# Kernel tuning notes

Hardware: AMD Instinct MI355X
Metric: run time of the kernel (lower is better)

## Reference

```python
import jax, jax.numpy as jnp
import numpy as np

# JetBlock dims
B, T, HID = 2, 2048, 2048
H, DK, DV = 16, 128, 128
W = 4                      # dynamic short-conv kernel size
GEN_IN = 2 * H * DK        # kernel generator conditioned on concat(q, k)
GEN_HID = H * DV
EPS_NORM = 1e-6
EPS_L2 = 1e-12


def _silu(x):
    return x * jax.nn.sigmoid(x)


def setup_inputs() -> dict:
    key = jax.random.key(0)
    ks = jax.random.split(key, 12)
    s = 0.02
    return {
        "x": jax.random.normal(ks[0], (B, T, HID), jnp.float32),
        "Wq": jax.random.normal(ks[1], (HID, H * DK), jnp.float32) * s,
        "Wk": jax.random.normal(ks[2], (HID, H * DK), jnp.float32) * s,
        "Wv": jax.random.normal(ks[3], (HID, H * DV), jnp.float32) * s,
        "Wb": jax.random.normal(ks[4], (HID, H), jnp.float32) * s,
        "Wa": jax.random.normal(ks[5], (HID, H), jnp.float32) * s,
        "dt_bias": jax.random.normal(ks[6], (H,), jnp.float32) * s,
        "A_log": jax.random.normal(ks[7], (H,), jnp.float32) * 0.5,
        "gen_w1": jax.random.normal(ks[8], (GEN_IN, GEN_HID), jnp.float32) * s,
        "gen_w2": jax.random.normal(ks[9], (GEN_HID, H * DV * W), jnp.float32) * s,
        "gen_b2": jnp.zeros((H * DV * W,), jnp.float32),
        "norm_weight": jnp.ones((DV,), jnp.float32),
        "Wg": jax.random.normal(ks[10], (HID, H * DV), jnp.float32) * s,
        "Wo": jax.random.normal(ks[11], (H * DV, HID), jnp.float32) * s,
    }


def reference(x, Wq, Wk, Wv, Wb, Wa, dt_bias, A_log, gen_w1, gen_w2, gen_b2,
              norm_weight, Wg, Wo):
    # projections
    q = (x @ Wq).reshape(B, T, H, DK)
    k = (x @ Wk).reshape(B, T, H, DK)
    v = x @ Wv  # [B, T, H*DV]

    # dynamic short convolution on v, kernels generated from concat(q, k)
    gi = jnp.concatenate([q.reshape(B, T, -1), k.reshape(B, T, -1)], axis=-1)
    kern = (_silu(gi @ gen_w1) @ gen_w2 + gen_b2).reshape(B, T, H * DV, W)
    vp = jnp.pad(v, ((0, 0), (W - 1, 0), (0, 0)))  # causal left pad
    # out[t, d] = sum_w kern[t, d, w] * v[t - (W-1) + w, d]
    vconv = kern[..., 0] * vp[:, 0:T, :]
    for w in range(1, W):
        vconv = vconv + kern[..., w] * vp[:, w:w + T, :]
    v = _silu(vconv).reshape(B, T, H, DV)

    # gating params (gated-deltanet parameterization)
    beta = jax.nn.sigmoid(x @ Wb)                              # [B, T, H]
    g = -jnp.exp(A_log) * jax.nn.softplus(x @ Wa + dt_bias)    # log-space decay <= 0
    decay = jnp.exp(g)

    # qk l2 norm (F.normalize semantics)
    qn = q / jnp.maximum(jnp.linalg.norm(q, axis=-1, keepdims=True), EPS_L2)
    kn = k / jnp.maximum(jnp.linalg.norm(k, axis=-1, keepdims=True), EPS_L2)

    # gated delta rule recurrence (o_t reads state BEFORE the update, per source)
    def step(S, inps):
        q_t, k_t, v_t, g_t, b_t = inps
        o_t = jnp.einsum('bnkv,bnk->bnv', S, q_t)
        Sk = jnp.einsum('bnkv,bnk->bnv', S, k_t)
        delta = v_t - Sk
        S = g_t[..., None, None] * S + b_t[..., None, None] * (
            k_t[..., :, None] * delta[..., None, :])
        return S, o_t

    S0 = jnp.zeros((B, H, DK, DV), x.dtype)
    xs = (jnp.moveaxis(qn, 1, 0), jnp.moveaxis(kn, 1, 0), jnp.moveaxis(v, 1, 0),
          jnp.moveaxis(decay, 1, 0), jnp.moveaxis(beta, 1, 0))
    _, o = jax.lax.scan(step, S0, xs)           # o: [T, B, H, DV]
    o = jnp.moveaxis(o, 0, 1)                   # [B, T, H, DV]

    # gated RMSNorm per head, then output projection
    gate = (x @ Wg).reshape(B, T, H, DV)
    rms = o * jax.lax.rsqrt(jnp.mean(o * o, axis=-1, keepdims=True) + EPS_NORM)
    o = rms * norm_weight * _silu(gate)
    return o.reshape(B, T, H * DV) @ Wo
```

## Files before the change

### kernel.cpp

```cpp
#include <hip/hip_runtime.h>
#include <hip/hip_bf16.h>


typedef _Float16 v8h __attribute__((ext_vector_type(8)));
typedef _Float16 v4h __attribute__((ext_vector_type(4)));
typedef _Float16 v2h __attribute__((ext_vector_type(2)));
typedef float    v4f __attribute__((ext_vector_type(4)));

__device__ __forceinline__ void gload16(const void* g, void* l) {
  __builtin_amdgcn_global_load_lds(
      (const __attribute__((address_space(1))) unsigned int*)g,
      (__attribute__((address_space(3))) unsigned int*)l, 16, 0, 0);
}

__global__ __launch_bounds__(256)
void transpose_cast(const float* __restrict__ src, _Float16* __restrict__ dst,
                    int R, int C)
{
  __shared__ float tile[32][33];
  int c0 = blockIdx.x * 32, r0 = blockIdx.y * 32;
  int tx = threadIdx.x & 31, ty = threadIdx.x >> 5;
  #pragma unroll
  for (int i = 0; i < 32; i += 8)
    tile[ty + i][tx] = src[(size_t)(r0 + ty + i) * C + c0 + tx];
  __syncthreads();
  #pragma unroll
  for (int i = 0; i < 32; i += 8)
    dst[(size_t)(c0 + ty + i) * R + r0 + tx] = (_Float16)tile[tx][ty + i];
}

__global__ __launch_bounds__(256)
void cast_f32_f16(const float* __restrict__ src, _Float16* __restrict__ dst, int n4)
{
  int i = blockIdx.x * 256 + threadIdx.x;
  if (i >= n4) return;
  float4 v = ((const float4*)src)[i];
  v4h h = {(_Float16)v.x, (_Float16)v.y, (_Float16)v.z, (_Float16)v.w};
  *(v4h*)&dst[4 * (size_t)i] = h;
}

template<int MODE>
__global__ __launch_bounds__(512, 2)
void gemm256(const _Float16* __restrict__ A, const _Float16* __restrict__ Bt,
             void* __restrict__ Cout, const float* __restrict__ bias,
             int M, int N, int K)
{
  __shared__ _Float16 lds[65536];
  const int tid  = threadIdx.x;
  const int lane = tid & 63;
  const int wid  = tid >> 6;
  const int wm   = wid >> 2;
  const int wn   = wid & 3;
  const int l16  = lane & 15;
  const int q8   = (lane >> 4) * 8;
  const int swzx = (l16 & 7) << 3;

  const int nbx = N >> 8;
  const int cpx = gridDim.x >> 3;
  const int swz = (blockIdx.x & 7) * cpx + (blockIdx.x >> 3);
  const int bm0 = (swz / nbx) << 8;
  const int bn0 = (swz % nbx) << 8;

  const _Float16* Abase = A  + (size_t)bm0 * K;
  const _Float16* Bbase = Bt + (size_t)bn0 * K;

  const int r0 = tid >> 3;
  const int cs = ((tid & 7) * 8) ^ ((r0 & 7) << 3);

#define SLOTA(par, half) (lds + ((par) * 2 + (half)) * 8192)
#define SLOTB(par, half) (lds + 32768 + ((par) * 2 + (half)) * 8192)
#define STAGE(basep, kt, slot) do {                                        \
    _Float16* sst_ = (slot);                                               \
    gload16((basep) + (size_t)r0 * K + (kt) + cs, sst_ + tid * 8);         \
    gload16((basep) + (size_t)(r0 + 64) * K + (kt) + cs,                   \
            sst_ + 4096 + tid * 8);                                        \
  } while (0)
#define LOADA(par, mh) do {                                                \
    const _Float16* sld_ = SLOTA(par, mh);                                 \
    _Pragma("unroll")                                                      \
    for (int ks = 0; ks < 2; ks++)                                         \
      _Pragma("unroll")                                                    \
      for (int mi = 0; mi < 4; mi++)                                       \
        af[ks][mi] = *(const v8h*)&sld_[(wm * 64 + mi * 16 + l16) * 64 +   \
                                        ((ks * 32 + q8) ^ swzx)];          \
  } while (0)
#define LOADB(par, nh) do {                                                \
    const _Float16* sld_ = SLOTB(par, nh);                                 \
    _Pragma("unroll")                                                      \
    for (int ks = 0; ks < 2; ks++)                                         \
      _Pragma("unroll")                                                    \
      for (int ni = 0; ni < 2; ni++)                                       \
        bf[ks][ni] = *(const v8h*)&sld_[(wn * 32 + ni * 16 + l16) * 64 +   \
                                        ((ks * 32 + q8) ^ swzx)];          \
  } while (0)
#define MMAC(mh, nh) do {                                                  \
    __builtin_amdgcn_s_setprio(1);                                         \
    _Pragma("unroll")                                                      \
    for (int ks = 0; ks < 2; ks++)                                         \
      _Pragma("unroll")                                                    \
      for (int mi = 0; mi < 4; mi++)                                       \
        _Pragma("unroll")                                                  \
        for (int ni = 0; ni < 2; ni++)                                     \
          acc[mh][mi][nh][ni] = __builtin_amdgcn_mfma_f32_16x16x32_f16(    \
              af[ks][mi], bf[ks][ni], acc[mh][mi][nh][ni], 0, 0, 0);       \
    __builtin_amdgcn_s_setprio(0);                                         \
  } while (0)

  v4f acc[2][4][2][2];
  #pragma unroll
  for (int mh = 0; mh < 2; mh++)
    #pragma unroll
    for (int mi = 0; mi < 4; mi++)
      #pragma unroll
      for (int nh = 0; nh < 2; nh++)
        #pragma unroll
        for (int ni = 0; ni < 2; ni++)
          acc[mh][mi][nh][ni] = v4f{0.f, 0.f, 0.f, 0.f};
  v8h af[2][4], bf[2][2];

  const int nt = K >> 6;

  STAGE(Abase,                   0,  SLOTA(0, 0));
  STAGE(Bbase,                   0,  SLOTB(0, 0));
  STAGE(Abase + (size_t)128 * K, 0,  SLOTA(0, 1));
  STAGE(Bbase + (size_t)128 * K, 0,  SLOTB(0, 1));
  STAGE(Abase,                   64, SLOTA(1, 0));
  STAGE(Bbase + (size_t)128 * K, 64, SLOTB(1, 1));
  asm volatile("s_waitcnt vmcnt(4)" ::: "memory");
  __builtin_amdgcn_s_barrier();

  for (int T = 0; T < nt; T++) {
    const int par = T & 1;
    const int kt1 = (T + 1) << 6;
    const int kt2 = (T + 2) << 6;
    LOADA(par, 0);
    LOADB(par, 0);
    if (T + 1 < nt) STAGE(Abase + (size_t)128 * K, kt1, SLOTA(par ^ 1, 1));
    __builtin_amdgcn_s_barrier();
    MMAC(0, 0);
    __builtin_amdgcn_s_barrier();
    LOADB(par, 1);
    if (T + 1 < nt) STAGE(Bbase, kt1, SLOTB(par ^ 1, 0));
    __builtin_amdgcn_s_barrier();
    MMAC(0, 1);
    __builtin_amdgcn_s_barrier();
    LOADA(par, 1);
    if (T + 2 < nt) STAGE(Abase, kt2, SLOTA(par, 0));
    __builtin_amdgcn_s_barrier();
    MMAC(1, 1);
    __builtin_amdgcn_s_barrier();
    LOADB(par, 0);
    if (T + 2 < nt) STAGE(Bbase + (size_t)128 * K, kt2, SLOTB(par, 1));
    __builtin_amdgcn_s_barrier();
    MMAC(1, 0);
    if (T + 2 < nt) { asm volatile("s_waitcnt vmcnt(4)" ::: "memory"); }
    else            { asm volatile("s_waitcnt vmcnt(0)" ::: "memory"); }
    __builtin_amdgcn_s_barrier();
  }

  const int q4 = (lane >> 4) * 4;
  #pragma unroll
  for (int mh = 0; mh < 2; mh++) {
    #pragma unroll
    for (int mi = 0; mi < 4; mi++) {
      #pragma unroll
      for (int nh = 0; nh < 2; nh++) {
        #pragma unroll
        for (int ni = 0; ni < 2; ni++) {
          const int gn = bn0 + nh * 128 + wn * 32 + ni * 16 + l16;
          #pragma unroll
          for (int r = 0; r < 4; r++) {
            const int gm = bm0 + mh * 128 + wm * 64 + mi * 16 + q4 + r;
            float val = acc[mh][mi][nh][ni][r];
            size_t offc = (size_t)gm * N + gn;
            if (MODE == 0) {
              ((float*)Cout)[offc] = val;
            } else if (MODE == 1) {
              float s = val / (1.0f + expf(-val));
              ((_Float16*)Cout)[offc] = (_Float16)s;
            } else if (MODE == 2) {
              float s = val + bias[gn];
              ((_Float16*)Cout)[offc] = (_Float16)s;
            } else {
              ((_Float16*)Cout)[offc] = (_Float16)val;
            }
          }
        }
      }
    }
  }
#undef SLOTA
#undef SLOTB
#undef STAGE
#undef LOADA
#undef LOADB
#undef MMAC
}

__global__ __launch_bounds__(256)
void conv_silu(const _Float16* __restrict__ vg, const _Float16* __restrict__ kernc,
               float* __restrict__ vprime, int chunk)
{
  int idx = blockIdx.x * 256 + threadIdx.x;
  int btl = idx >> 11;
  int d   = idx & 2047;
  int btg = chunk * 2048 + btl;
  v4h kv = *(const v4h*)&kernc[(size_t)btl * 8192 + d * 4];
  float kw0 = (float)kv[0], kw1 = (float)kv[1], kw2 = (float)kv[2], kw3 = (float)kv[3];
  const _Float16* vcol = vg + d;
  float acc = kw3 * (float)vcol[(size_t)btg * 4096];
  if (btl >= 1) acc += kw2 * (float)vcol[(size_t)(btg - 1) * 4096];
  if (btl >= 2) acc += kw1 * (float)vcol[(size_t)(btg - 2) * 4096];
  if (btl >= 3) acc += kw0 * (float)vcol[(size_t)(btg - 3) * 4096];
  vprime[(size_t)btg * 2048 + d] = acc / (1.0f + expf(-acc));
}

__global__ __launch_bounds__(256)
void beta_decay(const float* __restrict__ x, const float* __restrict__ Wb,
                const float* __restrict__ Wa, const float* __restrict__ dt_bias,
                const float* __restrict__ A_log,
                float* __restrict__ beta, float* __restrict__ glog)
{
  __shared__ float xs[2048];
  __shared__ float red[8][32];
  int row = blockIdx.x;
  int tid = threadIdx.x;
  for (int i = tid; i < 2048; i += 256) xs[i] = x[(size_t)row * 2048 + i];
  __syncthreads();
  int j = tid & 31, kg = tid >> 5;
  const float* W = (j < 16) ? Wb : Wa;
  int jj = j & 15;
  float acc = 0.f;
  int k0 = kg * 256;
  for (int k = k0; k < k0 + 256; k++) acc += xs[k] * W[(size_t)k * 16 + jj];
  red[kg][j] = acc;
  __syncthreads();
  if (tid < 32) {
    float s = 0.f;
    #pragma unroll
    for (int g2 = 0; g2 < 8; g2++) s += red[g2][tid];
    int hh = tid & 15;
    if (tid < 16) {
      beta[(size_t)row * 16 + hh] = 1.0f / (1.0f + expf(-s));
    } else {
      float tt = s + dt_bias[hh];
      float sp = (tt > 20.f) ? tt : log1pf(expf(tt));
      glog[(size_t)row * 16 + hh] = -expf(A_log[hh]) * sp;
    }
  }
}

__global__ __launch_bounds__(256)
void recurrence_seg(const _Float16* __restrict__ gi,
                    const float* __restrict__ vprime,
                    const float* __restrict__ betab,
                    const float* __restrict__ glogb,
                    float* __restrict__ o,
                    float* __restrict__ Send,
                    _Float16* __restrict__ obasis)
{
  __shared__ _Float16 Q16[32][136];
  __shared__ _Float16 K16[32][136];
  __shared__ _Float16 KT16[2][128][40];
  __shared__ _Float16 St16[64][136];
  __shared__ float V32[32][68];
  __shared__ float W0L[32][65];
  __shared__ float O0L[32][65];
  __shared__ float At32[32][32];
  __shared__ _Float16 B16[32][40];
  __shared__ _Float16 Ut16[64][40];
  __shared__ _Float16 Utp16[64][40];
  __shared__ float lgA[2][32], lgm1A[2][32], gm1E[2][32], bGA[2][32],
                   psA[2][32], betA[2][32], p31A[2];

  const int tid  = threadIdx.x;
  const int wid  = tid >> 6;
  const int lane = tid & 63;
  const int l16  = lane & 15;
  const int q8   = (lane >> 4) * 8;
  const int q4   = (lane >> 4) * 4;
  const int rg   = lane >> 4;
  const int wc   = wid * 16 + l16;

  const int role = blockIdx.x >> 6;
  const int blk  = blockIdx.x & 63;
  const int dvh  = blk & 1;
  const int h    = (blk >> 1) & 15;
  const int b    = blk >> 5;
  const int tbase = (role == 0) ? 0 : 1024;
  const bool basis = (role == 2);

  const _Float16* gq = gi + (size_t)b * 2048 * 4096 + h * 128;
  const _Float16* gk = gq + 2048;
  const float* vsrc = vprime + (size_t)b * 2048 * 2048 + h * 128 + dvh * 64;
  float* ob = o + ((size_t)(b * 2048 + tbase) * 16 + h) * 128 + dvh * 64;
  _Float16* obb = obasis + ((size_t)b * 1024 * 16 + h) * 128 + dvh * 64;

  const int sr  = tid >> 3;
  const int sc8 = tid & 7;
  const int c0  = sc8 * 16;
  const int ktsw = (tid & 3) << 3;

  v4f sfr[8];
  #pragma unroll
  for (int tn = 0; tn < 8; tn++) {
    #pragma unroll
    for (int fr = 0; fr < 4; fr++)
      sfr[tn][fr] = (basis && (tn * 16 + l16) == (dvh * 64 + wid * 16 + q4 + fr))
                        ? 1.f : 0.f;
  }

  v8h pq0, pq1, pk0, pk1;
  float4 pv0 = {0.f, 0.f, 0.f, 0.f}, pv1 = {0.f, 0.f, 0.f, 0.f};
  float pg = 0.f, pb = 0.f;

  auto stage_regs = [&](int t0) {
    pq0 = *(const v8h*)(gq + (size_t)(t0 + sr) * 4096 + c0);
    pq1 = *(const v8h*)(gq + (size_t)(t0 + sr) * 4096 + c0 + 8);
    pk0 = *(const v8h*)(gk + (size_t)(t0 + sr) * 4096 + c0);
    pk1 = *(const v8h*)(gk + (size_t)(t0 + sr) * 4096 + c0 + 8);
    if (!basis) {
      pv0 = *(const float4*)(vsrc + (size_t)(t0 + sr) * 2048 + sc8 * 8);
      pv1 = *(const float4*)(vsrc + (size_t)(t0 + sr) * 2048 + sc8 * 8 + 4);
    }
    if (tid < 32) {
      size_t bt_ = (size_t)(b * 2048 + t0 + tid) * 16 + h;
      pg = glogb[bt_];
      pb = betab[bt_];
    }
  };

  auto write_stage = [&](int pn) {
    float qf[16], kf[16];
    #pragma unroll
    for (int m = 0; m < 8; m++) {
      qf[m] = (float)pq0[m]; qf[m + 8] = (float)pq1[m];
      kf[m] = (float)pk0[m]; kf[m + 8] = (float)pk1[m];
    }
    float ssq = 0.f, ssk = 0.f;
    #pragma unroll
    for (int m = 0; m < 16; m++) { ssq += qf[m] * qf[m]; ssk += kf[m] * kf[m]; }
    ssq += __shfl_xor(ssq, 1); ssq += __shfl_xor(ssq, 2); ssq += __shfl_xor(ssq, 4);
    ssk += __shfl_xor(ssk, 1); ssk += __shfl_xor(ssk, 2); ssk += __shfl_xor(ssk, 4);
    float iq = 1.0f / fmaxf(sqrtf(ssq), 1e-12f);
    float ik = 1.0f / fmaxf(sqrtf(ssk), 1e-12f);
    v8h qo0, qo1, ko0, ko1;
    #pragma unroll
    for (int m = 0; m < 8; m++) {
      qo0[m] = (_Float16)(qf[m] * iq); qo1[m] = (_Float16)(qf[m + 8] * iq);
      ko0[m] = (_Float16)(kf[m] * ik); ko1[m] = (_Float16)(kf[m + 8] * ik);
    }
    *(v8h*)&Q16[sr][c0]     = qo0;
    *(v8h*)&Q16[sr][c0 + 8] = qo1;
    *(v8h*)&K16[sr][c0]     = ko0;
    *(v8h*)&K16[sr][c0 + 8] = ko1;
    #pragma unroll
    for (int m = 0; m < 8; m++) {
      KT16[pn][c0 + m][sr ^ ktsw]     = ko0[m];
      KT16[pn][c0 + 8 + m][sr ^ ktsw] = ko1[m];
    }
    *(float4*)&V32[sr][sc8 * 8]     = pv0;
    *(float4*)&V32[sr][sc8 * 8 + 4] = pv1;
    if (tid < 32) {
      float s = pg;
      #pragma unroll
      for (int d = 1; d < 32; d <<= 1) {
        float t = __shfl_up(s, d, 64);
        if (lane >= d) s += t;
      }
      float lg31 = __shfl(s, 31, 64);
      float lgm1 = s - pg;
      lgA[pn][lane]   = s;
      lgm1A[pn][lane] = lgm1;
      float g1 = expf(lgm1);
      gm1E[pn][lane]  = g1;
      bGA[pn][lane]   = pb * g1;
      psA[pn][lane]   = expf(lg31 - s);
      betA[pn][lane]  = pb;
      if (lane == 0) p31A[pn] = expf(lg31);
    }
  };

  stage_regs(tbase);
  for (int i = tid; i < 64 * 136; i += 256) {
    int r_ = i / 136, cc_ = i - r_ * 136;
    (&St16[0][0])[i] =
        (basis && cc_ == dvh * 64 + r_) ? (_Float16)1.f : (_Float16)0.f;
  }
  write_stage(0);
  __syncthreads();

  const v4f zf = {0.f, 0.f, 0.f, 0.f};

  for (int c = 0; c < 32; c++) {
    const int par = c & 1;

    if (c < 31) { stage_regs(tbase + (c + 1) * 32); __builtin_amdgcn_sched_barrier(0); }

    v4f kkf = zf, qkf = zf, w0f0 = zf, w0f1 = zf, o0f0 = zf, o0f1 = zf;
    {
      const int ai = (wid >> 1) * 16 + l16;
      const int bj = (wid & 1) * 16 + l16;
      #pragma unroll
      for (int ks = 0; ks < 4; ks++) {
        const int ko = ks * 32 + q8;
        v8h bs  = *(const v8h*)&St16[wid * 16 + l16][ko];
        v8h ak0 = *(const v8h*)&K16[l16][ko];
        v8h ak1 = *(const v8h*)&K16[16 + l16][ko];
        v8h aq0 = *(const v8h*)&Q16[l16][ko];
        v8h aq1 = *(const v8h*)&Q16[16 + l16][ko];
        w0f0 = __builtin_amdgcn_mfma_f32_16x16x32_f16(ak0, bs, w0f0, 0, 0, 0);
        w0f1 = __builtin_amdgcn_mfma_f32_16x16x32_f16(ak1, bs, w0f1, 0, 0, 0);
        o0f0 = __builtin_amdgcn_mfma_f32_16x16x32_f16(aq0, bs, o0f0, 0, 0, 0);
        o0f1 = __builtin_amdgcn_mfma_f32_16x16x32_f16(aq1, bs, o0f1, 0, 0, 0);
        v8h akk = *(const v8h*)&K16[ai][ko];
        v8h aqq = *(const v8h*)&Q16[ai][ko];
        v8h bkk = *(const v8h*)&K16[bj][ko];
        kkf = __builtin_amdgcn_mfma_f32_16x16x32_f16(akk, bkk, kkf, 0, 0, 0);
        qkf = __builtin_amdgcn_mfma_f32_16x16x32_f16(aqq, bkk, qkf, 0, 0, 0);
      }
    }
    {
      const int i0 = (wid >> 1) * 16, j = (wid & 1) * 16 + l16;
      #pragma unroll
      for (int fr = 0; fr < 4; fr++) {
        const int i = i0 + q4 + fr;
        float ex = expf(fminf(lgm1A[par][i] - lgA[par][j], 0.f));
        const bool lt = (j < i);
        At32[j][i] = lt ? betA[par][i] * ex * kkf[fr] : 0.f;
        B16[i][j]  = lt ? (_Float16)(ex * qkf[fr]) : (_Float16)0.f;
      }
      #pragma unroll
      for (int fr = 0; fr < 4; fr++) {
        W0L[q4 + fr][wid * 16 + l16]      = w0f0[fr];
        W0L[16 + q4 + fr][wid * 16 + l16] = w0f1[fr];
        O0L[q4 + fr][wid * 16 + l16]      = o0f0[fr];
        O0L[16 + q4 + fr][wid * 16 + l16] = o0f1[fr];
      }
    }
    __syncthreads();

    float ru[8];
    #pragma unroll
    for (int jj = 0; jj < 8; jj++) {
      const int row = rg * 8 + jj;
      ru[jj] = betA[par][row] * V32[row][wc] - bGA[par][row] * W0L[row][wc];
    }
    #pragma unroll
    for (int j = 0; j < 32; j++) {
      float uj = __shfl(ru[j & 7], (j >> 3) * 16 + l16, 64);
      const v4f a0 = *(const v4f*)&At32[j][rg * 8];
      const v4f a1 = *(const v4f*)&At32[j][rg * 8 + 4];
      ru[0] -= a0[0] * uj; ru[1] -= a0[1] * uj;
      ru[2] -= a0[2] * uj; ru[3] -= a0[3] * uj;
      ru[4] -= a1[0] * uj; ru[5] -= a1[1] * uj;
      ru[6] -= a1[2] * uj; ru[7] -= a1[3] * uj;
    }
    {
      v8h uo, upo;
      #pragma unroll
      for (int jj = 0; jj < 8; jj++) {
        uo[jj]  = (_Float16)ru[jj];
        upo[jj] = (_Float16)(ru[jj] * psA[par][rg * 8 + jj]);
      }
      *(v8h*)&Ut16[wc][rg * 8]  = uo;
      *(v8h*)&Utp16[wc][rg * 8] = upo;
    }
    __syncthreads();

    {
      v8h bu = *(const v8h*)&Ut16[wid * 16 + l16][q8];
      #pragma unroll
      for (int t2i = 0; t2i < 2; t2i++) {
        v8h a = *(const v8h*)&B16[t2i * 16 + l16][q8];
        v4f d = __builtin_amdgcn_mfma_f32_16x16x32_f16(a, bu, zf, 0, 0, 0);
        #pragma unroll
        for (int fr = 0; fr < 4; fr++) {
          const int i = t2i * 16 + q4 + fr;
          const int cc = wid * 16 + l16;
          float val = gm1E[par][i] * O0L[i][cc] + d[fr];
          size_t off = (size_t)(c * 32 + i) * 2048 + cc;
          if (basis) obb[off] = (_Float16)val;
          else       ob[off] = val;
        }
      }
      const float p31 = p31A[par];
      v8h ua = *(const v8h*)&Utp16[wid * 16 + l16][q8];
      #pragma unroll
      for (int tn = 0; tn < 8; tn++) {
        v8h bk = *(const v8h*)&KT16[par][tn * 16 + l16][q8 ^ ((tn & 3) << 3)];
        v4f sc = {sfr[tn][0] * p31, sfr[tn][1] * p31,
                  sfr[tn][2] * p31, sfr[tn][3] * p31};
        sfr[tn] = __builtin_amdgcn_mfma_f32_16x16x32_f16(ua, bk, sc, 0, 0, 0);
        #pragma unroll
        for (int fr = 0; fr < 4; fr++)
          St16[wid * 16 + q4 + fr][tn * 16 + l16] = (_Float16)sfr[tn][fr];
      }
    }
    if (c < 31) write_stage((c + 1) & 1);
    __syncthreads();
  }

  if (role == 0) {
    float* sg = Send + (size_t)(b * 16 + h) * 128 * 128;
    #pragma unroll
    for (int tn = 0; tn < 8; tn++)
      #pragma unroll
      for (int fr = 0; fr < 4; fr++)
        sg[(size_t)(dvh * 64 + wid * 16 + q4 + fr) * 128 + tn * 16 + l16] =
            sfr[tn][fr];
  }
}

__global__ __launch_bounds__(256)
void apply_basis(const _Float16* __restrict__ obasis,
                 const float* __restrict__ Send,
                 float* __restrict__ o)
{
  __shared__ _Float16 Ao[128][136];
  __shared__ _Float16 Bs[128][136];
  const int bh = blockIdx.x & 31;
  const int tt = blockIdx.x >> 5;
  const int b = bh >> 4, h = bh & 15;
  const int tid = threadIdx.x;
  const int wid = tid >> 6, lane = tid & 63;
  const int l16 = lane & 15, q8 = (lane >> 4) * 8, q4 = (lane >> 4) * 4;

  const _Float16* asrc = obasis + ((size_t)(b * 1024 + tt * 128) * 16 + h) * 128;
  for (int i = tid; i < 128 * 16; i += 256) {
    int r = i >> 4, c8 = (i & 15) * 8;
    *(v8h*)&Ao[r][c8] = *(const v8h*)(asrc + (size_t)r * 2048 + c8);
  }
  const float* ssrc = Send + (size_t)bh * 128 * 128;
  for (int i = tid; i < 128 * 16; i += 256) {
    int r = i >> 4, c8 = (i & 15) * 8;
    v8h tmp;
    #pragma unroll
    for (int m = 0; m < 8; m++) tmp[m] = (_Float16)ssrc[(size_t)r * 128 + c8 + m];
    *(v8h*)&Bs[r][c8] = tmp;
  }
  __syncthreads();

  v4f acc[2][8];
  #pragma unroll
  for (int rt = 0; rt < 2; rt++)
    #pragma unroll
    for (int ct = 0; ct < 8; ct++) acc[rt][ct] = v4f{0.f, 0.f, 0.f, 0.f};
  #pragma unroll
  for (int ks = 0; ks < 4; ks++) {
    v8h af0 = *(const v8h*)&Ao[wid * 32 + l16][ks * 32 + q8];
    v8h af1 = *(const v8h*)&Ao[wid * 32 + 16 + l16][ks * 32 + q8];
    #pragma unroll
    for (int ct = 0; ct < 8; ct++) {
      v8h bf = *(const v8h*)&Bs[ct * 16 + l16][ks * 32 + q8];
      acc[0][ct] = __builtin_amdgcn_mfma_f32_16x16x32_f16(af0, bf, acc[0][ct], 0, 0, 0);
      acc[1][ct] = __builtin_amdgcn_mfma_f32_16x16x32_f16(af1, bf, acc[1][ct], 0, 0, 0);
    }
  }
  float* obp = o + ((size_t)(b * 2048 + 1024 + tt * 128) * 16 + h) * 128;
  #pragma unroll
  for (int rt = 0; rt < 2; rt++) {
    #pragma unroll
    for (int ct = 0; ct < 8; ct++) {
      #pragma unroll
      for (int fr = 0; fr < 4; fr++) {
        const int row = wid * 32 + rt * 16 + q4 + fr;
        const int col = ct * 16 + l16;
        obp[(size_t)row * 2048 + col] += acc[rt][ct][fr];
      }
    }
  }
}

__global__ __launch_bounds__(256)
void rms_gate(const float* __restrict__ o, const _Float16* __restrict__ vg,
              const float* __restrict__ normw, _Float16* __restrict__ yh)
{
  int task = blockIdx.x * 4 + (threadIdx.x >> 6);
  int lane = threadIdx.x & 63;
  int bt = task >> 4, h = task & 15;
  float2 v = *(const float2*)(o + (size_t)task * 128 + lane * 2);
  float ss = v.x * v.x + v.y * v.y;
  #pragma unroll
  for (int m = 1; m < 64; m <<= 1) ss += __shfl_xor(ss, m);
  float r = rsqrtf(ss * (1.0f / 128.0f) + 1e-6f);
  v2h gt2 = *(const v2h*)(vg + (size_t)bt * 4096 + 2048 + h * 128 + lane * 2);
  float gx = (float)gt2[0], gy = (float)gt2[1];
  float2 nw = *(const float2*)(normw + lane * 2);
  float g0 = gx / (1.0f + expf(-gx));
  float g1 = gy / (1.0f + expf(-gy));
  v2h outp = {(_Float16)(v.x * r * nw.x * g0), (_Float16)(v.y * r * nw.y * g1)};
  *(v2h*)(yh + (size_t)bt * 2048 + h * 128 + lane * 2) = outp;
}

extern "C" void kernel_launch(void* const* d_in, const int* in_sizes, int n_in,
                              void* d_out, int out_size, void* d_ws, size_t ws_size,
                              hipStream_t stream)
{
  (void)in_sizes; (void)n_in; (void)out_size;
  const float* x       = (const float*)d_in[0];
  const float* Wq      = (const float*)d_in[1];
  const float* Wk      = (const float*)d_in[2];
  const float* Wv      = (const float*)d_in[3];
  const float* Wb      = (const float*)d_in[4];
  const float* Wa      = (const float*)d_in[5];
  const float* dt_bias = (const float*)d_in[6];
  const float* A_log   = (const float*)d_in[7];
  const float* gen_w1  = (const float*)d_in[8];
  const float* gen_w2  = (const float*)d_in[9];
  const float* gen_b2  = (const float*)d_in[10];
  const float* normw   = (const float*)d_in[11];
  const float* Wg      = (const float*)d_in[12];
  const float* Wo      = (const float*)d_in[13];

  const size_t SZ_GI   = 4096ull * 4096 * 2;
  const size_t SZ_VG   = 4096ull * 4096 * 2;
  const size_t SZ_WT   = 8192ull * 2048 * 2;
  const size_t SZ_D    = 4096ull * 2048 * 2;
  const size_t SZ_KC   = 2048ull * 8192 * 2;
  const size_t SZ_VP   = 4096ull * 2048 * 4;
  const size_t SZ_SM   = 4096ull * 16 * 4;
  const size_t NEEDED = SZ_GI + SZ_VG + SZ_WT + SZ_D + SZ_KC + SZ_VP + 2 * SZ_SM;
  if (ws_size < NEEDED) return;

  char* w = (char*)d_ws;
  _Float16* gi     = (_Float16*)(w);
  _Float16* vg     = (_Float16*)(w + SZ_GI);
  _Float16* Wt     = (_Float16*)(w + SZ_GI + SZ_VG);
  char*     Dreg   =            (w + SZ_GI + SZ_VG + SZ_WT);
  _Float16* kernc  = (_Float16*)(w + SZ_GI + SZ_VG + SZ_WT + SZ_D);
  float*    vprime = (float*)   (w + SZ_GI + SZ_VG + SZ_WT + SZ_D + SZ_KC);
  float*    betab  = (float*)   (w + SZ_GI + SZ_VG + SZ_WT + SZ_D + SZ_KC + SZ_VP);
  float*    glogb  = (float*)   (w + SZ_GI + SZ_VG + SZ_WT + SZ_D + SZ_KC + SZ_VP + SZ_SM);
  _Float16* xh  = (_Float16*)Dreg;
  _Float16* hid = (_Float16*)Dreg;
  _Float16* yh  = (_Float16*)Dreg;
  float* obuf = (float*)d_out;

  _Float16* obasis = (_Float16*)(w + SZ_GI + SZ_VG);
  float*    Send   = (float*)   (w + SZ_GI + SZ_VG + 2ull * 1024 * 16 * 128 * 2);

  dim3 blk(256);
  dim3 blk512(512);

  cast_f32_f16<<<8192, blk, 0, stream>>>(x, xh, 4096 * 2048 / 4);

  transpose_cast<<<dim3(64, 64), blk, 0, stream>>>(Wq, Wt, 2048, 2048);
  transpose_cast<<<dim3(64, 64), blk, 0, stream>>>(Wk, Wt + 2048 * 2048, 2048, 2048);
  gemm256<3><<<256, blk512, 0, stream>>>(xh, Wt, gi, nullptr, 4096, 4096, 2048);

  transpose_cast<<<dim3(64, 64), blk, 0, stream>>>(Wv, Wt, 2048, 2048);
  transpose_cast<<<dim3(64, 64), blk, 0, stream>>>(Wg, Wt + 2048 * 2048, 2048, 2048);
  gemm256<3><<<256, blk512, 0, stream>>>(xh, Wt, vg, nullptr, 4096, 4096, 2048);

  transpose_cast<<<dim3(64, 128), blk, 0, stream>>>(gen_w1, Wt, 4096, 2048);
  gemm256<1><<<128, blk512, 0, stream>>>(gi, Wt, hid, nullptr, 4096, 2048, 4096);

  transpose_cast<<<dim3(256, 64), blk, 0, stream>>>(gen_w2, Wt, 2048, 8192);
  for (int chunk = 0; chunk < 2; chunk++) {
    gemm256<2><<<256, blk512, 0, stream>>>(hid + (size_t)chunk * 2048 * 2048, Wt,
                                           kernc, gen_b2, 2048, 8192, 2048);
    conv_silu<<<16384, blk, 0, stream>>>(vg, kernc, vprime, chunk);
  }

  beta_decay<<<4096, blk, 0, stream>>>(x, Wb, Wa, dt_bias, A_log, betab, glogb);
  recurrence_seg<<<192, blk, 0, stream>>>(gi, vprime, betab, glogb, obuf,
                                          Send, obasis);
  apply_basis<<<256, blk, 0, stream>>>(obasis, Send, obuf);
  rms_gate<<<16384, blk, 0, stream>>>(obuf, vg, normw, yh);

  transpose_cast<<<dim3(64, 64), blk, 0, stream>>>(Wo, Wt, 2048, 2048);
  gemm256<0><<<128, blk512, 0, stream>>>(yh, Wt, (float*)d_out, nullptr, 4096, 2048, 2048);
}
```

Measured before the change: 968.9 us.

## Split delta-rule recurrence into four time segments with state composition kernel

```diff
diff --git a/kernel.cpp b/kernel.cpp
--- a/kernel.cpp
+++ b/kernel.cpp
@@ -11,6 +11,10 @@
   __builtin_amdgcn_global_load_lds(
       (const __attribute__((address_space(1))) unsigned int*)g,
       (__attribute__((address_space(3))) unsigned int*)l, 16, 0, 0);
+}
+
+__device__ __forceinline__ int sw64(int r, int c) {
+  return (c & 7) | ((((c >> 3) ^ (r & 7) ^ (r >> 3)) & 7) << 3);
 }
 
 __global__ __launch_bounds__(256)
@@ -250,26 +254,26 @@
   }
 }
 
+#define SEGC 16
 __global__ __launch_bounds__(256)
 void recurrence_seg(const _Float16* __restrict__ gi,
                     const float* __restrict__ vprime,
                     const float* __restrict__ betab,
                     const float* __restrict__ glogb,
                     float* __restrict__ o,
-                    float* __restrict__ Send,
+                    float* __restrict__ Sloc,
+                    _Float16* __restrict__ Mst,
                     _Float16* __restrict__ obasis)
 {
   __shared__ _Float16 Q16[32][136];
   __shared__ _Float16 K16[32][136];
-  __shared__ _Float16 KT16[2][128][40];
+  __shared__ _Float16 KT16[128][40];
   __shared__ _Float16 St16[64][136];
-  __shared__ float V32[32][68];
-  __shared__ float W0L[32][65];
-  __shared__ float O0L[32][65];
-  __shared__ float At32[32][32];
+  __shared__ _Float16 V16[32][64];
+  __shared__ _Float16 W16[32][64];
+  __shared__ float At32[32][36];
   __shared__ _Float16 B16[32][40];
   __shared__ _Float16 Ut16[64][40];
-  __shared__ _Float16 Utp16[64][40];
   __shared__ float lgA[2][32], lgm1A[2][32], gm1E[2][32], bGA[2][32],
                    psA[2][32], betA[2][32], p31A[2];
 
@@ -287,19 +291,22 @@
   const int dvh  = blk & 1;
   const int h    = (blk >> 1) & 15;
   const int b    = blk >> 5;
-  const int tbase = (role == 0) ? 0 : 1024;
-  const bool basis = (role == 2);
+  const bool basis = (role >= 4);
+  const int seg  = basis ? (role - 3) : role;
+  const int tbase = seg * 512;
+  const int bh = b * 16 + h;
 
   const _Float16* gq = gi + (size_t)b * 2048 * 4096 + h * 128;
   const _Float16* gk = gq + 2048;
   const float* vsrc = vprime + (size_t)b * 2048 * 2048 + h * 128 + dvh * 64;
   float* ob = o + ((size_t)(b * 2048 + tbase) * 16 + h) * 128 + dvh * 64;
-  _Float16* obb = obasis + ((size_t)b * 1024 * 16 + h) * 128 + dvh * 64;
+  _Float16* obb = obasis + (size_t)(seg - 1) * 2097152
+                  + ((size_t)b * 512 * 16 + h) * 128 + dvh * 64;
 
   const int sr  = tid >> 3;
   const int sc8 = tid & 7;
   const int c0  = sc8 * 16;
-  const int ktsw = (tid & 3) << 3;
+  const int ktsw = (sc8 & 3) << 3;
 
   v4f sfr[8];
   #pragma unroll
@@ -311,6 +318,7 @@
   }
 
   v8h pq0, pq1, pk0, pk1;
+  v8h kon0, kon1;
   float4 pv0 = {0.f, 0.f, 0.f, 0.f}, pv1 = {0.f, 0.f, 0.f, 0.f};
   float pg = 0.f, pb = 0.f;
 
@@ -354,13 +362,13 @@
     *(v8h*)&Q16[sr][c0 + 8] = qo1;
     *(v8h*)&K16[sr][c0]     = ko0;
     *(v8h*)&K16[sr][c0 + 8] = ko1;
-    #pragma unroll
-    for (int m = 0; m < 8; m++) {
-      KT16[pn][c0 + m][sr ^ ktsw]     = ko0[m];
-      KT16[pn][c0 + 8 + m][sr ^ ktsw] = ko1[m];
-    }
-    *(float4*)&V32[sr][sc8 * 8]     = pv0;
-    *(float4*)&V32[sr][sc8 * 8 + 4] = pv1;
+    kon0 = ko0; kon1 = ko1;
+    {
+      int swb = (sc8 ^ (sr & 7) ^ (sr >> 3)) & 7;
+      v8h vo = {(_Float16)pv0.x, (_Float16)pv0.y, (_Float16)pv0.z, (_Float16)pv0.w,
+                (_Float16)pv1.x, (_Float16)pv1.y, (_Float16)pv1.z, (_Float16)pv1.w};
+      *(v8h*)&V16[sr][swb * 8] = vo;
+    }
     if (tid < 32) {
       float s = pg;
       #pragma unroll
@@ -392,10 +400,19 @@
 
   const v4f zf = {0.f, 0.f, 0.f, 0.f};
 
-  for (int c = 0; c < 32; c++) {
+  for (int c = 0; c < SEGC; c++) {
     const int par = c & 1;
 
-    if (c < 31) { stage_regs(tbase + (c + 1) * 32); __builtin_amdgcn_sched_barrier(0); }
+    if (c + 1 < SEGC) stage_regs(tbase + (c + 1) * 32);
+    {
+      float ps = psA[par][sr];
+      #pragma unroll
+      for (int m = 0; m < 8; m++) {
+        KT16[c0 + m][sr ^ ktsw]     = (_Float16)((float)kon0[m] * ps);
+        KT16[c0 + 8 + m][sr ^ ktsw] = (_Float16)((float)kon1[m] * ps);
+      }
+    }
+    __builtin_amdgcn_sched_barrier(0);
 
     v4f kkf = zf, qkf = zf, w0f0 = zf, w0f1 = zf, o0f0 = zf, o0f1 = zf;
     {
@@ -430,12 +447,12 @@
         At32[j][i] = lt ? betA[par][i] * ex * kkf[fr] : 0.f;
         B16[i][j]  = lt ? (_Float16)(ex * qkf[fr]) : (_Float16)0.f;
       }
+      const int cc = wid * 16 + l16;
       #pragma unroll
       for (int fr = 0; fr < 4; fr++) {
-        W0L[q4 + fr][wid * 16 + l16]      = w0f0[fr];
-        W0L[16 + q4 + fr][wid * 16 + l16] = w0f1[fr];
-        O0L[q4 + fr][wid * 16 + l16]      = o0f0[fr];
-        O0L[16 + q4 + fr][wid * 16 + l16] = o0f1[fr];
+        const int r1 = q4 + fr, r2 = 16 + q4 + fr;
+        W16[r1][sw64(r1, cc)] = (_Float16)w0f0[fr];
+        W16[r2][sw64(r2, cc)] = (_Float16)w0f1[fr];
       }
     }
     __syncthreads();
@@ -444,7 +461,10 @@
     #pragma unroll
     for (int jj = 0; jj < 8; jj++) {
       const int row = rg * 8 + jj;
-      ru[jj] = betA[par][row] * V32[row][wc] - bGA[par][row] * W0L[row][wc];
+      const int sc_ = sw64(row, wc);
+      float vv = (float)V16[row][sc_];
+      float wv = (float)W16[row][sc_];
+      ru[jj] = betA[par][row] * vv - bGA[par][row] * wv;
     }
     #pragma unroll
     for (int j = 0; j < 32; j++) {
@@ -457,14 +477,10 @@
       ru[6] -= a1[2] * uj; ru[7] -= a1[3] * uj;
     }
     {
-      v8h uo, upo;
-      #pragma unroll
-      for (int jj = 0; jj < 8; jj++) {
-        uo[jj]  = (_Float16)ru[jj];
-        upo[jj] = (_Float16)(ru[jj] * psA[par][rg * 8 + jj]);
-      }
-      *(v8h*)&Ut16[wc][rg * 8]  = uo;
-      *(v8h*)&Utp16[wc][rg * 8] = upo;
+      v8h uo;
+      #pragma unroll
+      for (int jj = 0; jj < 8; jj++) uo[jj] = (_Float16)ru[jj];
+      *(v8h*)&Ut16[wc][rg * 8] = uo;
     }
     __syncthreads();
 
@@ -478,31 +494,31 @@
         for (int fr = 0; fr < 4; fr++) {
           const int i = t2i * 16 + q4 + fr;
           const int cc = wid * 16 + l16;
-          float val = gm1E[par][i] * O0L[i][cc] + d[fr];
+          float o0 = (t2i == 0) ? o0f0[fr] : o0f1[fr];
+          float val = gm1E[par][i] * o0 + d[fr];
           size_t off = (size_t)(c * 32 + i) * 2048 + cc;
           if (basis) obb[off] = (_Float16)val;
           else       ob[off] = val;
         }
       }
       const float p31 = p31A[par];
-      v8h ua = *(const v8h*)&Utp16[wid * 16 + l16][q8];
       #pragma unroll
       for (int tn = 0; tn < 8; tn++) {
-        v8h bk = *(const v8h*)&KT16[par][tn * 16 + l16][q8 ^ ((tn & 3) << 3)];
+        v8h bk = *(const v8h*)&KT16[tn * 16 + l16][q8 ^ ((tn & 3) << 3)];
         v4f sc = {sfr[tn][0] * p31, sfr[tn][1] * p31,
                   sfr[tn][2] * p31, sfr[tn][3] * p31};
-        sfr[tn] = __builtin_amdgcn_mfma_f32_16x16x32_f16(ua, bk, sc, 0, 0, 0);
+        sfr[tn] = __builtin_amdgcn_mfma_f32_16x16x32_f16(bu, bk, sc, 0, 0, 0);
         #pragma unroll
         for (int fr = 0; fr < 4; fr++)
           St16[wid * 16 + q4 + fr][tn * 16 + l16] = (_Float16)sfr[tn][fr];
       }
     }
-    if (c < 31) write_stage((c + 1) & 1);
+    if (c + 1 < SEGC) write_stage((c + 1) & 1);
     __syncthreads();
   }
 
-  if (role == 0) {
-    float* sg = Send + (size_t)(b * 16 + h) * 128 * 128;
+  if (!basis && seg < 3) {
+    float* sg = Sloc + ((size_t)seg * 32 + bh) * 16384;
     #pragma unroll
     for (int tn = 0; tn < 8; tn++)
       #pragma unroll
@@ -510,34 +526,117 @@
         sg[(size_t)(dvh * 64 + wid * 16 + q4 + fr) * 128 + tn * 16 + l16] =
             sfr[tn][fr];
   }
+  if (basis && seg <= 2) {
+    _Float16* mg = Mst + ((size_t)(seg - 1) * 32 + bh) * 16384;
+    #pragma unroll
+    for (int tn = 0; tn < 8; tn++)
+      #pragma unroll
+      for (int fr = 0; fr < 4; fr++)
+        mg[(size_t)(dvh * 64 + wid * 16 + q4 + fr) * 128 + tn * 16 + l16] =
+            (_Float16)sfr[tn][fr];
+  }
+}
+
+__global__ __launch_bounds__(256)
+void compose_state(const float* __restrict__ Sloc, const _Float16* __restrict__ Mst,
+                   _Float16* __restrict__ SinS)
+{
+  __shared__ _Float16 AL[128][136];
+  __shared__ _Float16 BL[128][136];
+  const int bh = blockIdx.x;
+  const int tid = threadIdx.x;
+  const int wid = tid >> 6, lane = tid & 63;
+  const int l16 = lane & 15, q8 = (lane >> 4) * 8, q4 = (lane >> 4) * 4;
+
+  {
+    const float* s0 = Sloc + (size_t)bh * 16384;
+    _Float16* d0 = SinS + (size_t)bh * 16384;
+    for (int i = tid; i < 2048; i += 256) {
+      int r = i >> 4, c8 = (i & 15) * 8;
+      v8h t;
+      #pragma unroll
+      for (int m = 0; m < 8; m++) t[m] = (_Float16)s0[(size_t)r * 128 + c8 + m];
+      *(v8h*)&AL[r][c8] = t;
+      *(v8h*)(d0 + (size_t)r * 128 + c8) = t;
+    }
+  }
+  __syncthreads();
+
+  for (int st = 0; st < 2; st++) {
+    const _Float16* ms = Mst + ((size_t)st * 32 + bh) * 16384;
+    for (int i = tid; i < 2048; i += 256) {
+      int r = i >> 4, c8 = (i & 15) * 8;
+      v8h t = *(const v8h*)(ms + (size_t)r * 128 + c8);
+      #pragma unroll
+      for (int m = 0; m < 8; m++) BL[c8 + m][r] = t[m];
+    }
+    __syncthreads();
+
+    v4f acc[2][8];
+    #pragma unroll
+    for (int rt = 0; rt < 2; rt++)
+      #pragma unroll
+      for (int ct = 0; ct < 8; ct++) acc[rt][ct] = v4f{0.f, 0.f, 0.f, 0.f};
+    #pragma unroll
+    for (int ks = 0; ks < 4; ks++) {
+      v8h a0 = *(const v8h*)&AL[wid * 32 + l16][ks * 32 + q8];
+      v8h a1 = *(const v8h*)&AL[wid * 32 + 16 + l16][ks * 32 + q8];
+      #pragma unroll
+      for (int ct = 0; ct < 8; ct++) {
+        v8h bfv = *(const v8h*)&BL[ct * 16 + l16][ks * 32 + q8];
+        acc[0][ct] = __builtin_amdgcn_mfma_f32_16x16x32_f16(a0, bfv, acc[0][ct], 0, 0, 0);
+        acc[1][ct] = __builtin_amdgcn_mfma_f32_16x16x32_f16(a1, bfv, acc[1][ct], 0, 0, 0);
+      }
+    }
+    __syncthreads();
+
+    const float* sn = Sloc + ((size_t)(st + 1) * 32 + bh) * 16384;
+    _Float16* dn = SinS + ((size_t)(st + 1) * 32 + bh) * 16384;
+    #pragma unroll
+    for (int rt = 0; rt < 2; rt++) {
+      #pragma unroll
+      for (int ct = 0; ct < 8; ct++) {
+        #pragma unroll
+        for (int fr = 0; fr < 4; fr++) {
+          const int row = wid * 32 + rt * 16 + q4 + fr;
+          const int col = ct * 16 + l16;
+          float val = acc[rt][ct][fr] + sn[(size_t)row * 128 + col];
+          _Float16 hv = (_Float16)val;
+          AL[row][col] = hv;
+          dn[(size_t)row * 128 + col] = hv;
+        }
+      }
+    }
+    __syncthreads();
+  }
 }
 
 __global__ __launch_bounds__(256)
 void apply_basis(const _Float16* __restrict__ obasis,
-                 const float* __restrict__ Send,
+                 const _Float16* __restrict__ SinS,
                  float* __restrict__ o)
 {
   __shared__ _Float16 Ao[128][136];
   __shared__ _Float16 Bs[128][136];
-  const int bh = blockIdx.x & 31;
-  const int tt = blockIdx.x >> 5;
+  const int ss = blockIdx.x >> 7;
+  const int rem = blockIdx.x & 127;
+  const int tt = rem >> 5;
+  const int bh = rem & 31;
   const int b = bh >> 4, h = bh & 15;
   const int tid = threadIdx.x;
   const int wid = tid >> 6, lane = tid & 63;
   const int l16 = lane & 15, q8 = (lane >> 4) * 8, q4 = (lane >> 4) * 4;
 
-  const _Float16* asrc = obasis + ((size_t)(b * 1024 + tt * 128) * 16 + h) * 128;
-  for (int i = tid; i < 128 * 16; i += 256) {
+  const _Float16* asrc = obasis + (size_t)ss * 2097152
+                         + ((size_t)(b * 512 + tt * 128) * 16 + h) * 128;
+  for (int i = tid; i < 2048; i += 256) {
     int r = i >> 4, c8 = (i & 15) * 8;
     *(v8h*)&Ao[r][c8] = *(const v8h*)(asrc + (size_t)r * 2048 + c8);
   }
-  const float* ssrc = Send + (size_t)bh * 128 * 128;
-  for (int i = tid; i < 128 * 16; i += 256) {
+  const _Float16* ssrc = SinS + ((size_t)ss * 32 + bh) * 16384;
+  for (int i = tid; i < 2048; i += 256) {
     int r = i >> 4, c8 = (i & 15) * 8;
-    v8h tmp;
-    #pragma unroll
-    for (int m = 0; m < 8; m++) tmp[m] = (_Float16)ssrc[(size_t)r * 128 + c8 + m];
-    *(v8h*)&Bs[r][c8] = tmp;
+    *(v8h*)&Bs[r][c8] = *(const v8h*)(ssrc + (size_t)r * 128 + c8);
   }
   __syncthreads();
 
@@ -557,7 +656,7 @@
       acc[1][ct] = __builtin_amdgcn_mfma_f32_16x16x32_f16(af1, bf, acc[1][ct], 0, 0, 0);
     }
   }
-  float* obp = o + ((size_t)(b * 2048 + 1024 + tt * 128) * 16 + h) * 128;
+  float* obp = o + ((size_t)(b * 2048 + (ss + 1) * 512 + tt * 128) * 16 + h) * 128;
   #pragma unroll
   for (int rt = 0; rt < 2; rt++) {
     #pragma unroll
@@ -638,7 +737,9 @@
   float* obuf = (float*)d_out;
 
   _Float16* obasis = (_Float16*)(w + SZ_GI + SZ_VG);
-  float*    Send   = (float*)   (w + SZ_GI + SZ_VG + 2ull * 1024 * 16 * 128 * 2);
+  float*    Sloc   = (float*)   (w + SZ_GI + SZ_VG + 12582912ull);
+  _Float16* MstB   = (_Float16*)(w + SZ_GI + SZ_VG + 12582912ull + 6291456ull);
+  _Float16* SinS   = (_Float16*)(w + SZ_GI + SZ_VG + 12582912ull + 6291456ull + 2097152ull);
 
   dim3 blk(256);
   dim3 blk512(512);
@@ -664,9 +765,10 @@
   }
 
   beta_decay<<<4096, blk, 0, stream>>>(x, Wb, Wa, dt_bias, A_log, betab, glogb);
-  recurrence_seg<<<192, blk, 0, stream>>>(gi, vprime, betab, glogb, obuf,
-                                          Send, obasis);
-  apply_basis<<<256, blk, 0, stream>>>(obasis, Send, obuf);
+  recurrence_seg<<<448, blk, 0, stream>>>(gi, vprime, betab, glogb, obuf,
+                                          Sloc, MstB, obasis);
+  compose_state<<<32, blk, 0, stream>>>(Sloc, MstB, SinS);
+  apply_basis<<<384, blk, 0, stream>>>(obasis, SinS, obuf);
   rms_gate<<<16384, blk, 0, stream>>>(obuf, vg, normw, yh);
 
   transpose_cast<<<dim3(64, 64), blk, 0, stream>>>(Wo, Wt, 2048, 2048);
```

After: 976.4 us. Within noise of the previous version (+0.8%).
